# Kernel tuning notes

Measured on AMD Instinct MI355X. Metric: run time of the kernel, lower is better.

## Reference

```python
import jax, jax.numpy as jnp
import numpy as np

B, S, D, H, DFF, K = 16, 1024, 1024, 16, 4096, 3


def setup_inputs() -> dict:
    key = jax.random.key(0)
    ks = jax.random.split(key, 8)
    f = lambda k, sh: jax.random.normal(k, sh, jnp.float32) * 0.02
    return dict(
        x=jax.random.normal(ks[0], (B, S, D), jnp.float32),
        mask=jnp.ones((B, 1, S), jnp.int32),
        alpha1=jnp.ones((D,), jnp.float32), bias1=jnp.zeros((D,), jnp.float32),
        alpha2=jnp.ones((D,), jnp.float32), bias2=jnp.zeros((D,), jnp.float32),
        W_l1=f(ks[1], (D, 2 * D)), b_l1=jnp.zeros((2 * D,), jnp.float32),
        conv_w=f(ks[2], (H, K)),
        W_l2=f(ks[3], (D, D)), b_l2=jnp.zeros((D,), jnp.float32),
        W_ff1=f(ks[4], (D, DFF)), b_ff1=jnp.zeros((DFF,), jnp.float32),
        W_ff2=f(ks[5], (DFF, D)), b_ff2=jnp.zeros((D,), jnp.float32),
    )


def _norm(x, alpha, bias, eps=1e-6):
    # Norm: alpha * (x - mean) / (std + eps) + bias, torch std is unbiased (ddof=1)
    mu = x.mean(-1, keepdims=True)
    sd = x.std(-1, keepdims=True, ddof=1)
    return alpha * (x - mu) / (sd + eps) + bias


def _lightconv(x, conv_w):
    # x: [B, S, C]; conv_w: [H, K] softmax-normalized over K; channels in a head share kernel
    C = x.shape[-1]
    w = jax.nn.softmax(conv_w, axis=-1)              # [H, K]
    wk = jnp.repeat(w, C // H, axis=0)[:, None, :]   # [C, 1, K] depthwise kernel
    y = jax.lax.conv_general_dilated(
        x.transpose(0, 2, 1), wk, (1,), [(K // 2, (K - 1) // 2)],
        dimension_numbers=('NCH', 'OIH', 'NCH'), feature_group_count=C)
    return y.transpose(0, 2, 1)


def reference(x, mask, alpha1, bias1, alpha2, bias2, W_l1, b_l1, conv_w,
              W_l2, b_l2, W_ff1, b_ff1, W_ff2, b_ff2):
    # --- lightweight-conv sublayer ---
    res = x
    h = _norm(x, alpha1, bias1)
    h = h @ W_l1 + b_l1                         # [B,S,2C]
    a, b = jnp.split(h, 2, axis=-1)
    h = a * jax.nn.sigmoid(b)                   # GLU -> [B,S,C]
    cm = mask[:, -1, :][:, :, None]             # [B,S,1]
    h = jnp.where(cm == 0, 0.0, h)
    h = _lightconv(h, conv_w)
    h = h @ W_l2 + b_l2
    x = res + h
    # --- FFN sublayer ---
    res = x
    h = _norm(x, alpha2, bias2)
    h = jax.nn.relu(h @ W_ff1 + b_ff1) @ W_ff2 + b_ff2
    return res + h
```

## Files before the change

kernel.cpp:

```cpp
#include <hip/hip_runtime.h>

typedef unsigned short ushort_t;
typedef __attribute__((ext_vector_type(8))) short s8v;
typedef __attribute__((ext_vector_type(4))) float f4v;

__device__ __forceinline__ float b2f(ushort_t h) {
    union { unsigned u; float f; } c; c.u = ((unsigned)h) << 16; return c.f;
}
__device__ __forceinline__ ushort_t f2b(float f) {
    union { float f; unsigned u; } c; c.f = f;
    unsigned u = c.u;
    return (ushort_t)((u + 0x7fffu + ((u >> 16) & 1u)) >> 16);
}

__device__ __forceinline__ void glds16(const void* g, void* l) {
    __builtin_amdgcn_global_load_lds(
        (const __attribute__((address_space(1))) void*)g,
        (__attribute__((address_space(3))) void*)l, 16, 0, 0);
}

template <int PERM>
__global__ __launch_bounds__(256) void trans_k(const float* __restrict__ W,
                                               ushort_t* __restrict__ Wt,
                                               int K, int N) {
    __shared__ float tile[64][65];
    int k0 = blockIdx.x * 64, n0 = blockIdx.y * 64;
    int t = threadIdx.x;
    int c = t & 63, r4 = t >> 6;
#pragma unroll
    for (int i = 0; i < 16; ++i) {
        int r = i * 4 + r4;
        tile[r][c] = W[(size_t)(k0 + r) * N + n0 + c];
    }
    __syncthreads();
#pragma unroll
    for (int i = 0; i < 16; ++i) {
        int r = i * 4 + r4;
        int s = n0 + r;
        int d;
        if (PERM) {
            int a = (s < 1024);
            int s2 = a ? s : s - 1024;
            d = ((s2 >> 7) << 8) + (a ? 0 : 128) + (s2 & 127);
        } else {
            d = s;
        }
        Wt[(size_t)d * K + k0 + c] = f2b(tile[c][r]);
    }
}

__global__ __launch_bounds__(256) void norm_k(const float* __restrict__ x,
                                              const float* __restrict__ al,
                                              const float* __restrict__ be,
                                              ushort_t* __restrict__ out) {
    int row = blockIdx.x;
    const float4* xr = (const float4*)(x + (size_t)row * 1024);
    float4 v = xr[threadIdx.x];
    float s = v.x + v.y + v.z + v.w;
    float q = v.x * v.x + v.y * v.y + v.z * v.z + v.w * v.w;
#pragma unroll
    for (int o = 32; o > 0; o >>= 1) {
        s += __shfl_down(s, o);
        q += __shfl_down(q, o);
    }
    __shared__ float ss[4], qq[4];
    int lane = threadIdx.x & 63, wv = threadIdx.x >> 6;
    if (lane == 0) { ss[wv] = s; qq[wv] = q; }
    __syncthreads();
    s = ss[0] + ss[1] + ss[2] + ss[3];
    q = qq[0] + qq[1] + qq[2] + qq[3];
    float mu = s * (1.f / 1024.f);
    float var = (q - 1024.f * mu * mu) * (1.f / 1023.f);
    var = fmaxf(var, 0.f);
    float inv = 1.f / (sqrtf(var) + 1e-6f);
    float4 a4 = ((const float4*)al)[threadIdx.x];
    float4 b4 = ((const float4*)be)[threadIdx.x];
    ushort4 o4;
    o4.x = f2b(a4.x * (v.x - mu) * inv + b4.x);
    o4.y = f2b(a4.y * (v.y - mu) * inv + b4.y);
    o4.z = f2b(a4.z * (v.z - mu) * inv + b4.z);
    o4.w = f2b(a4.w * (v.w - mu) * inv + b4.w);
    ((ushort4*)(out + (size_t)row * 1024))[threadIdx.x] = o4;
}

__global__ __launch_bounds__(256) void conv_k(const ushort_t* __restrict__ g,
                                              const float* __restrict__ cw,
                                              ushort_t* __restrict__ out) {
    int i = blockIdx.x * 256 + threadIdx.x;
    int row = i >> 7;
    int cc = (i & 127) << 3;
    int s = row & 1023;
    int head = cc >> 6;
    float w0 = cw[head * 3 + 0], w1 = cw[head * 3 + 1], w2 = cw[head * 3 + 2];
    float mx = fmaxf(w0, fmaxf(w1, w2));
    float e0 = __expf(w0 - mx), e1 = __expf(w1 - mx), e2 = __expf(w2 - mx);
    float inv = 1.f / (e0 + e1 + e2);
    w0 = e0 * inv; w1 = e1 * inv; w2 = e2 * inv;
    size_t base = (size_t)row * 1024 + cc;
    s8v z = {0, 0, 0, 0, 0, 0, 0, 0};
    s8v vm = (s > 0)    ? *(const s8v*)(g + base - 1024) : z;
    s8v v0 = *(const s8v*)(g + base);
    s8v vp = (s < 1023) ? *(const s8v*)(g + base + 1024) : z;
    s8v ov;
#pragma unroll
    for (int j = 0; j < 8; ++j) {
        float r = w0 * b2f((ushort_t)vm[j]) + w1 * b2f((ushort_t)v0[j]) +
                  w2 * b2f((ushort_t)vp[j]);
        ov[j] = (short)f2b(r);
    }
    *(s8v*)(out + base) = ov;
}

template <int EPI>
__global__ __launch_bounds__(512, 1) void gemm_k(const ushort_t* __restrict__ A,
                                                 const ushort_t* __restrict__ Bt,
                                                 const float* __restrict__ bias,
                                                 const int* __restrict__ maskp,
                                                 const float* res, float* outf,
                                                 ushort_t* outb, int N, int K) {
    __shared__ char smem[131072] __attribute__((aligned(128)));
    const int NBN = N >> 8;
    const int per = gridDim.x >> 3;
    const int tt = (blockIdx.x & 7) * per + (blockIdx.x >> 3);
    const int gw = NBN << 3;
    const int g = tt / gw;
    const int rem = tt - g * gw;
    const int bm = (g << 3) + (rem & 7);
    const int bn = rem >> 3;

    const int t = threadIdx.x;
    const int l = t & 63, w = t >> 6;
    const int wm = w >> 2, wn = w & 3;
    const int lr = l & 15, lk = l >> 4;

    const int swzel = (((t & 3) ^ ((t >> 3) & 3)) << 3);
    const int r0 = t >> 2;
    const ushort_t* pA0 = A + (size_t)(bm * 256 + r0) * K + swzel;
    const ushort_t* pA1 = pA0 + (size_t)128 * K;
    const ushort_t* pB0 = Bt + (size_t)(bn * 256 + r0) * K + swzel;
    const ushort_t* pB1 = pB0 + (size_t)128 * K;

    const int fswz = ((lk ^ ((lr >> 1) & 3)) << 4);
    int aoff[8], boff[4];
#pragma unroll
    for (int m = 0; m < 8; ++m)
        aoff[m] = (wm * 128 + m * 16 + lr) * 64 + fswz;
#pragma unroll
    for (int n = 0; n < 4; ++n)
        boff[n] = 16384 + (wn * 64 + n * 16 + lr) * 64 + fswz;

    f4v acc[8][4];
#pragma unroll
    for (int m = 0; m < 8; ++m)
#pragma unroll
        for (int n = 0; n < 4; ++n) acc[m][n] = f4v{0.f, 0.f, 0.f, 0.f};

    const int NK = K >> 5;

#pragma unroll
    for (int p = 0; p < 3; ++p) {
        char* d = smem + p * 32768 + t * 16;
        glds16(pA0 + p * 32, d);
        glds16(pA1 + p * 32, d + 8192);
        glds16(pB0 + p * 32, d + 16384);
        glds16(pB1 + p * 32, d + 24576);
    }
    asm volatile("s_waitcnt vmcnt(8)");
    __builtin_amdgcn_s_barrier();
    __builtin_amdgcn_sched_barrier(0);

    s8v aL0[4], bF0[4], aL1[4], bF1[4], aH[4];
#pragma unroll
    for (int m = 0; m < 4; ++m) aL0[m] = *(const s8v*)(smem + aoff[m]);
#pragma unroll
    for (int n = 0; n < 4; ++n) bF0[n] = *(const s8v*)(smem + boff[n]);

#define KSTEP(I, CAL, CBF, NAL, NBF)                                           \
    {                                                                          \
        const int i_ = (I);                                                    \
        const char* cb_ = smem + (size_t)(i_ & 3) * 32768;                     \
        const char* nb_ = smem + (size_t)((i_ + 1) & 3) * 32768;               \
        int st_ = i_ + 3; if (st_ >= NK) st_ = NK - 1;                         \
        char* sd_ = smem + (size_t)((i_ + 3) & 3) * 32768 + t * 16;            \
        const int ko_ = st_ * 32;                                              \
        _Pragma("unroll")                                                      \
        for (int m = 0; m < 4; ++m) aH[m] = *(const s8v*)(cb_ + aoff[4 + m]);  \
        glds16(pA0 + ko_, sd_);                                                \
        glds16(pA1 + ko_, sd_ + 8192);                                         \
        glds16(pB0 + ko_, sd_ + 16384);                                        \
        glds16(pB1 + ko_, sd_ + 24576);                                        \
        __builtin_amdgcn_s_setprio(1);                                         \
        _Pragma("unroll")                                                      \
        for (int m = 0; m < 4; ++m)                                            \
            _Pragma("unroll")                                                  \
            for (int n = 0; n < 4; ++n)                                        \
                acc[m][n] = __builtin_amdgcn_mfma_f32_16x16x32_bf16(           \
                    CAL[m], CBF[n], acc[m][n], 0, 0, 0);                       \
        __builtin_amdgcn_s_setprio(0);                                         \
        __builtin_amdgcn_sched_barrier(0);                                     \
        asm volatile("s_waitcnt vmcnt(6)");                                    \
        __builtin_amdgcn_s_barrier();                                          \
        __builtin_amdgcn_sched_barrier(0);                                     \
        _Pragma("unroll")                                                      \
        for (int m = 0; m < 4; ++m) NAL[m] = *(const s8v*)(nb_ + aoff[m]);     \
        _Pragma("unroll")                                                      \
        for (int n = 0; n < 4; ++n) NBF[n] = *(const s8v*)(nb_ + boff[n]);     \
        __builtin_amdgcn_s_setprio(1);                                         \
        _Pragma("unroll")                                                      \
        for (int m = 0; m < 4; ++m)                                            \
            _Pragma("unroll")                                                  \
            for (int n = 0; n < 4; ++n)                                        \
                acc[4 + m][n] = __builtin_amdgcn_mfma_f32_16x16x32_bf16(       \
                    aH[m], CBF[n], acc[4 + m][n], 0, 0, 0);                    \
        __builtin_amdgcn_s_setprio(0);                                         \
    }

    for (int ii = 0; ii < NK; ii += 2) {
        KSTEP(ii, aL0, bF0, aL1, bF1);
        KSTEP(ii + 1, aL1, bF1, aL0, bF0);
    }
#undef KSTEP

    if (EPI == 1) {
#pragma unroll
        for (int n = 0; n < 4; ++n) {
            int gcol = bn * 256 + wn * 64 + n * 16 + lr;
            float bb = bias[gcol];
#pragma unroll
            for (int m = 0; m < 8; ++m) {
#pragma unroll
                for (int r = 0; r < 4; ++r) {
                    int grow = bm * 256 + wm * 128 + m * 16 + lk * 4 + r;
                    size_t oi = (size_t)grow * N + gcol;
                    outf[oi] = acc[m][n][r] + bb + res[oi];
                }
            }
        }
    } else {
        asm volatile("s_waitcnt vmcnt(0)" ::: "memory");
        __builtin_amdgcn_s_barrier();
        float bb4[4];
#pragma unroll
        for (int n = 0; n < 4; ++n) {
            int d = bn * 256 + wn * 64 + n * 16 + lr;
            int src = ((d >> 8) << 7) + (d & 127) + (((d >> 7) & 1) << 10);
            bb4[n] = bias[src];
        }
#pragma unroll
        for (int m = 0; m < 8; ++m)
#pragma unroll
            for (int n = 0; n < 4; ++n)
#pragma unroll
                for (int r = 0; r < 4; ++r) {
                    int row = wm * 128 + m * 16 + lk * 4 + r;
                    int colb = ((wn * 64 + n * 16 + lr) * 2) ^ ((row & 3) << 4);
                    *(ushort_t*)(smem + row * 512 + colb) =
                        f2b(acc[m][n][r] + bb4[n]);
                }
        __builtin_amdgcn_s_barrier();
#pragma unroll
        for (int s = 0; s < 8; ++s) {
            int row = s * 32 + (t >> 4);
            int abyt = row * 512 + (((t & 15) * 16) ^ ((row & 3) << 4));
            s8v av = *(const s8v*)(smem + abyt);
            s8v bv = *(const s8v*)(smem + abyt + 256);
            int grow = bm * 256 + row;
            float mval = (maskp[grow] == 0) ? 0.f : 1.f;
            s8v ov;
#pragma unroll
            for (int j = 0; j < 8; ++j) {
                float a = b2f((ushort_t)av[j]);
                float xx = b2f((ushort_t)bv[j]);
                ov[j] = (short)f2b(a * mval / (1.f + __expf(-xx)));
            }
            *(s8v*)(outb + (size_t)grow * (N >> 1) + bn * 128 + (t & 15) * 8) =
                ov;
        }
    }
}

template <int EPI>
__global__ __launch_bounds__(256, 1) void gemm4w_k(
    const ushort_t* __restrict__ A, const ushort_t* __restrict__ Bt,
    const float* __restrict__ bias, const float* res, float* outf,
    ushort_t* outb, int N, int K) {
    __shared__ char smem[131072] __attribute__((aligned(128)));
    const int NBN = N >> 8;
    const int per = gridDim.x >> 3;
    const int tt = (blockIdx.x & 7) * per + (blockIdx.x >> 3);
    const int gw = NBN << 3;
    const int g = tt / gw;
    const int rem = tt - g * gw;
    const int bm = (g << 3) + (rem & 7);
    const int bn = rem >> 3;

    const int t = threadIdx.x;
    const int l = t & 63, w = t >> 6;
    const int wm = w >> 1, wn = w & 1;
    const int lr = l & 15, lk = l >> 4;

    const int swzel = (((t & 3) ^ ((t >> 3) & 3)) << 3);
    const int r0 = t >> 2;
    const ushort_t* pA[4];
    const ushort_t* pB[4];
#pragma unroll
    for (int j = 0; j < 4; ++j) {
        pA[j] = A + (size_t)(bm * 256 + r0 + 64 * j) * K + swzel;
        pB[j] = Bt + (size_t)(bn * 256 + r0 + 64 * j) * K + swzel;
    }

    const int fswz = ((lk ^ ((lr >> 1) & 3)) << 4);
    int aoff[8], boff[8];
#pragma unroll
    for (int m = 0; m < 8; ++m) {
        aoff[m] = (wm * 128 + m * 16 + lr) * 64 + fswz;
        boff[m] = 16384 + (wn * 128 + m * 16 + lr) * 64 + fswz;
    }

    f4v acc[8][8];
#pragma unroll
    for (int m = 0; m < 8; ++m)
#pragma unroll
        for (int n = 0; n < 8; ++n) acc[m][n] = f4v{0.f, 0.f, 0.f, 0.f};

    const int NK = K >> 5;

#pragma unroll
    for (int p = 0; p < 3; ++p) {
        char* d = smem + p * 32768 + t * 16;
#pragma unroll
        for (int j = 0; j < 4; ++j) {
            glds16(pA[j] + p * 32, d + j * 4096);
            glds16(pB[j] + p * 32, d + 16384 + j * 4096);
        }
    }
    asm volatile("s_waitcnt vmcnt(16)");
    __builtin_amdgcn_s_barrier();
    __builtin_amdgcn_sched_barrier(0);

    for (int i = 0; i < NK; ++i) {
        const char* cb = smem + (size_t)(i & 3) * 32768;
        int st = i + 3; if (st >= NK) st = NK - 1;
        const int ko = st * 32;
        char* sd = smem + (size_t)((i + 3) & 3) * 32768 + t * 16;

#pragma unroll
        for (int j = 0; j < 4; ++j) {
            glds16(pA[j] + ko, sd + j * 4096);
            glds16(pB[j] + ko, sd + 16384 + j * 4096);
        }

        s8v aF[8], bF[8];
#pragma unroll
        for (int m = 0; m < 8; ++m) aF[m] = *(const s8v*)(cb + aoff[m]);
#pragma unroll
        for (int n = 0; n < 8; ++n) bF[n] = *(const s8v*)(cb + boff[n]);
        __builtin_amdgcn_s_setprio(1);
#pragma unroll
        for (int m = 0; m < 8; ++m)
#pragma unroll
            for (int n = 0; n < 8; ++n)
                acc[m][n] = __builtin_amdgcn_mfma_f32_16x16x32_bf16(
                    aF[m], bF[n], acc[m][n], 0, 0, 0);
        __builtin_amdgcn_s_setprio(0);

        __builtin_amdgcn_sched_barrier(0);
        asm volatile("s_waitcnt vmcnt(16)");
        __builtin_amdgcn_s_barrier();
        __builtin_amdgcn_sched_barrier(0);
    }

    if (EPI == 1) {
#pragma unroll
        for (int n = 0; n < 8; ++n) {
            int gcol = bn * 256 + wn * 128 + n * 16 + lr;
            float bb = bias[gcol];
#pragma unroll
            for (int m = 0; m < 8; ++m) {
#pragma unroll
                for (int r = 0; r < 4; ++r) {
                    int grow = bm * 256 + wm * 128 + m * 16 + lk * 4 + r;
                    size_t oi = (size_t)grow * N + gcol;
                    outf[oi] = acc[m][n][r] + bb + res[oi];
                }
            }
        }
    } else {
        asm volatile("s_waitcnt vmcnt(0)" ::: "memory");
        __builtin_amdgcn_s_barrier();
        float bb8[8];
#pragma unroll
        for (int n = 0; n < 8; ++n)
            bb8[n] = bias[bn * 256 + wn * 128 + n * 16 + lr];
#pragma unroll
        for (int m = 0; m < 8; ++m)
#pragma unroll
            for (int n = 0; n < 8; ++n)
#pragma unroll
                for (int r = 0; r < 4; ++r) {
                    int row = wm * 128 + m * 16 + lk * 4 + r;
                    int colb =
                        ((wn * 128 + n * 16 + lr) * 2) ^ ((row & 3) << 4);
                    *(ushort_t*)(smem + row * 512 + colb) =
                        f2b(fmaxf(acc[m][n][r] + bb8[n], 0.f));
                }
        __builtin_amdgcn_s_barrier();
#pragma unroll
        for (int s = 0; s < 32; ++s) {
            int row = s * 8 + (t >> 5);
            int byt = row * 512 + (((t & 31) * 16) ^ ((row & 3) << 4));
            int grow = bm * 256 + row;
            int gcol = bn * 256 + (t & 31) * 8;
            *(s8v*)(outb + (size_t)grow * N + gcol) = *(const s8v*)(smem + byt);
        }
    }
}

extern "C" void kernel_launch(void* const* d_in, const int* in_sizes, int n_in,
                              void* d_out, int out_size, void* d_ws, size_t ws_size,
                              hipStream_t stream) {
    const float* x      = (const float*)d_in[0];
    const int*   mask   = (const int*)d_in[1];
    const float* alpha1 = (const float*)d_in[2];
    const float* bias1  = (const float*)d_in[3];
    const float* alpha2 = (const float*)d_in[4];
    const float* bias2  = (const float*)d_in[5];
    const float* W_l1   = (const float*)d_in[6];
    const float* b_l1   = (const float*)d_in[7];
    const float* conv_w = (const float*)d_in[8];
    const float* W_l2   = (const float*)d_in[9];
    const float* b_l2   = (const float*)d_in[10];
    const float* W_ff1  = (const float*)d_in[11];
    const float* b_ff1  = (const float*)d_in[12];
    const float* W_ff2  = (const float*)d_in[13];
    const float* b_ff2  = (const float*)d_in[14];
    float* out = (float*)d_out;

    char* ws = (char*)d_ws;
    size_t off = 0;
    auto alloc = [&](size_t b) {
        char* p = ws + off;
        off += (b + 255) & ~(size_t)255;
        return p;
    };
    ushort_t* Wl1t  = (ushort_t*)alloc(2048ull * 1024 * 2);
    ushort_t* Wl2t  = (ushort_t*)alloc(1024ull * 1024 * 2);
    ushort_t* Wff1t = (ushort_t*)alloc(4096ull * 1024 * 2);
    ushort_t* Wff2t = (ushort_t*)alloc(1024ull * 4096 * 2);
    char* regA = alloc(134217728ull);
    ushort_t* B1 = (ushort_t*)alloc(33554432ull);
    ushort_t* C1 = (ushort_t*)alloc(33554432ull);
    ushort_t* G1 = (ushort_t*)regA;
    ushort_t* f1 = (ushort_t*)regA;

    const int R = 16384;

    trans_k<1><<<dim3(16, 32), 256, 0, stream>>>(W_l1, Wl1t, 1024, 2048);
    trans_k<0><<<dim3(16, 16), 256, 0, stream>>>(W_l2, Wl2t, 1024, 1024);
    trans_k<0><<<dim3(16, 64), 256, 0, stream>>>(W_ff1, Wff1t, 1024, 4096);
    trans_k<0><<<dim3(64, 16), 256, 0, stream>>>(W_ff2, Wff2t, 4096, 1024);

    norm_k<<<R, 256, 0, stream>>>(x, alpha1, bias1, B1);
    gemm_k<3><<<64 * 8, 512, 0, stream>>>(B1, Wl1t, b_l1, mask, nullptr,
                                          nullptr, G1, 2048, 1024);
    conv_k<<<8192, 256, 0, stream>>>(G1, conv_w, C1);
    gemm_k<1><<<64 * 4, 512, 0, stream>>>(C1, Wl2t, b_l2, nullptr, x, out,
                                          nullptr, 1024, 1024);

    norm_k<<<R, 256, 0, stream>>>(out, alpha2, bias2, B1);
    gemm4w_k<2><<<64 * 16, 256, 0, stream>>>(B1, Wff1t, b_ff1, nullptr,
                                             nullptr, f1, 4096, 1024);
    gemm4w_k<1><<<64 * 4, 256, 0, stream>>>(f1, Wff2t, b_ff2, out, out,
                                            nullptr, 1024, 4096);
}
```

Measured before the change: 609.2 us.

## Rewrite FFN GEMM as 8-wave ping-pong kernel with interleaved loads

```diff
diff --git a/kernel.cpp b/kernel.cpp
--- a/kernel.cpp
+++ b/kernel.cpp
@@ -280,7 +280,7 @@
 }
 
 template <int EPI>
-__global__ __launch_bounds__(256, 1) void gemm4w_k(
+__global__ __launch_bounds__(512, 1) void gemm8p_k(
     const ushort_t* __restrict__ A, const ushort_t* __restrict__ Bt,
     const float* __restrict__ bias, const float* res, float* outf,
     ushort_t* outb, int N, int K) {
@@ -296,90 +296,153 @@
 
     const int t = threadIdx.x;
     const int l = t & 63, w = t >> 6;
-    const int wm = w >> 1, wn = w & 1;
+    const int wm = w >> 2, wn = w & 3;
     const int lr = l & 15, lk = l >> 4;
-
-    const int swzel = (((t & 3) ^ ((t >> 3) & 3)) << 3);
-    const int r0 = t >> 2;
-    const ushort_t* pA[4];
-    const ushort_t* pB[4];
-#pragma unroll
-    for (int j = 0; j < 4; ++j) {
-        pA[j] = A + (size_t)(bm * 256 + r0 + 64 * j) * K + swzel;
-        pB[j] = Bt + (size_t)(bn * 256 + r0 + 64 * j) * K + swzel;
-    }
-
-    const int fswz = ((lk ^ ((lr >> 1) & 3)) << 4);
-    int aoff[8], boff[8];
-#pragma unroll
-    for (int m = 0; m < 8; ++m) {
-        aoff[m] = (wm * 128 + m * 16 + lr) * 64 + fswz;
-        boff[m] = 16384 + (wn * 128 + m * 16 + lr) * 64 + fswz;
-    }
-
-    f4v acc[8][8];
+    const int t16 = t * 16;
+
+    const int srcsl = (((t & 7) ^ ((t >> 3) & 7)) << 3);
+    const int rs = t >> 3;
+    const ushort_t* pAL0 = A + (size_t)(bm * 256 + rs) * K + srcsl;
+    const ushort_t* pAL1 = pAL0 + (size_t)64 * K;
+    const ushort_t* pAH0 = pAL0 + (size_t)128 * K;
+    const ushort_t* pAH1 = pAL0 + (size_t)192 * K;
+    const ushort_t* pBL0 = Bt + (size_t)(bn * 256 + rs) * K + srcsl;
+    const ushort_t* pBL1 = pBL0 + (size_t)64 * K;
+    const ushort_t* pBH0 = pBL0 + (size_t)128 * K;
+    const ushort_t* pBH1 = pBL0 + (size_t)192 * K;
+
+    const int rowA = (wm * 16 + lr) * 128;
+    const int rowB = (wn * 16 + lr) * 128;
+    int xk[2];
+#pragma unroll
+    for (int ks = 0; ks < 2; ++ks)
+        xk[ks] = (((ks * 4 + lk) ^ (lr & 7)) << 4);
+
+    f4v acc[8][4];
 #pragma unroll
     for (int m = 0; m < 8; ++m)
 #pragma unroll
-        for (int n = 0; n < 8; ++n) acc[m][n] = f4v{0.f, 0.f, 0.f, 0.f};
-
-    const int NK = K >> 5;
-
-#pragma unroll
-    for (int p = 0; p < 3; ++p) {
-        char* d = smem + p * 32768 + t * 16;
-#pragma unroll
-        for (int j = 0; j < 4; ++j) {
-            glds16(pA[j] + p * 32, d + j * 4096);
-            glds16(pB[j] + p * 32, d + 16384 + j * 4096);
-        }
-    }
-    asm volatile("s_waitcnt vmcnt(16)");
+        for (int n = 0; n < 4; ++n) acc[m][n] = f4v{0.f, 0.f, 0.f, 0.f};
+
+    const int NT = K >> 6;
+
+#pragma unroll
+    for (int p = 0; p < 2; ++p) {
+        char* b = smem + p * 65536 + t16;
+        const int ko = p * 64;
+        glds16(pAL0 + ko, b);
+        glds16(pAL1 + ko, b + 8192);
+        glds16(pBL0 + ko, b + 32768);
+        glds16(pBL1 + ko, b + 40960);
+        glds16(pBH0 + ko, b + 49152);
+        glds16(pBH1 + ko, b + 57344);
+        glds16(pAH0 + ko, b + 16384);
+        glds16(pAH1 + ko, b + 24576);
+    }
+    asm volatile("s_waitcnt vmcnt(8)");
     __builtin_amdgcn_s_barrier();
-    __builtin_amdgcn_sched_barrier(0);
-
-    for (int i = 0; i < NK; ++i) {
-        const char* cb = smem + (size_t)(i & 3) * 32768;
-        int st = i + 3; if (st >= NK) st = NK - 1;
-        const int ko = st * 32;
-        char* sd = smem + (size_t)((i + 3) & 3) * 32768 + t * 16;
-
-#pragma unroll
-        for (int j = 0; j < 4; ++j) {
-            glds16(pA[j] + ko, sd + j * 4096);
-            glds16(pB[j] + ko, sd + 16384 + j * 4096);
-        }
-
-        s8v aF[8], bF[8];
-#pragma unroll
-        for (int m = 0; m < 8; ++m) aF[m] = *(const s8v*)(cb + aoff[m]);
-#pragma unroll
-        for (int n = 0; n < 8; ++n) bF[n] = *(const s8v*)(cb + boff[n]);
-        __builtin_amdgcn_s_setprio(1);
-#pragma unroll
-        for (int m = 0; m < 8; ++m)
-#pragma unroll
-            for (int n = 0; n < 8; ++n)
-                acc[m][n] = __builtin_amdgcn_mfma_f32_16x16x32_bf16(
-                    aF[m], bF[n], acc[m][n], 0, 0, 0);
-        __builtin_amdgcn_s_setprio(0);
-
-        __builtin_amdgcn_sched_barrier(0);
-        asm volatile("s_waitcnt vmcnt(16)");
-        __builtin_amdgcn_s_barrier();
-        __builtin_amdgcn_sched_barrier(0);
-    }
+
+    s8v aR[4][2], bR[4][2];
+
+#define MFMAQ(MB, NB)                                                          \
+    _Pragma("unroll")                                                          \
+    for (int ks = 0; ks < 2; ++ks)                                             \
+        _Pragma("unroll")                                                      \
+        for (int m = 0; m < 4; ++m)                                            \
+            _Pragma("unroll")                                                  \
+            for (int n = 0; n < 2; ++n)                                        \
+                acc[(MB) + m][(NB) + n] =                                      \
+                    __builtin_amdgcn_mfma_f32_16x16x32_bf16(                   \
+                        aR[m][ks], bR[(NB) + n][ks],                           \
+                        acc[(MB) + m][(NB) + n], 0, 0, 0);
+
+#define KT(TI)                                                                 \
+    {                                                                          \
+        const int ti_ = (TI);                                                  \
+        const char* cb_ = smem + (size_t)(ti_ & 1) * 65536;                    \
+        char* sb_ = smem + (size_t)(ti_ & 1) * 65536;                          \
+        int st_ = ti_ + 2;                                                     \
+        if (st_ >= NT) st_ = NT - 2 + (ti_ & 1);                               \
+        const int ko_ = st_ * 64;                                              \
+                                                             \
+        _Pragma("unroll")                                                      \
+        for (int m = 0; m < 4; ++m)                                            \
+            _Pragma("unroll")                                                  \
+            for (int ks = 0; ks < 2; ++ks)                                     \
+                aR[m][ks] = *(const s8v*)(cb_ + m * 4096 + rowA + xk[ks]);     \
+        _Pragma("unroll")                                                      \
+        for (int n = 0; n < 2; ++n)                                            \
+            _Pragma("unroll")                                                  \
+            for (int ks = 0; ks < 2; ++ks)                                     \
+                bR[n][ks] =                                                    \
+                    *(const s8v*)(cb_ + 32768 + n * 8192 + rowB + xk[ks]);     \
+        asm volatile("s_waitcnt lgkmcnt(8)");                                  \
+        __builtin_amdgcn_s_barrier();                                          \
+        asm volatile("s_waitcnt lgkmcnt(0)");                                  \
+        __builtin_amdgcn_s_setprio(1);                                         \
+        MFMAQ(0, 0)                                                            \
+        __builtin_amdgcn_s_setprio(0);                                         \
+        __builtin_amdgcn_s_barrier();                                          \
+                                                             \
+        _Pragma("unroll")                                                      \
+        for (int n = 0; n < 2; ++n)                                            \
+            _Pragma("unroll")                                                  \
+            for (int ks = 0; ks < 2; ++ks)                                     \
+                bR[2 + n][ks] =                                                \
+                    *(const s8v*)(cb_ + 49152 + n * 8192 + rowB + xk[ks]);     \
+        glds16(pAL0 + ko_, sb_ + t16);                                         \
+        glds16(pAL1 + ko_, sb_ + 8192 + t16);                                  \
+        __builtin_amdgcn_s_barrier();                                          \
+        asm volatile("s_waitcnt lgkmcnt(0)");                                  \
+        __builtin_amdgcn_s_setprio(1);                                         \
+        MFMAQ(0, 2)                                                            \
+        __builtin_amdgcn_s_setprio(0);                                         \
+        __builtin_amdgcn_s_barrier();                                          \
+                                                             \
+        _Pragma("unroll")                                                      \
+        for (int m = 0; m < 4; ++m)                                            \
+            _Pragma("unroll")                                                  \
+            for (int ks = 0; ks < 2; ++ks)                                     \
+                aR[m][ks] =                                                    \
+                    *(const s8v*)(cb_ + 16384 + m * 4096 + rowA + xk[ks]);     \
+        glds16(pBL0 + ko_, sb_ + 32768 + t16);                                 \
+        glds16(pBL1 + ko_, sb_ + 40960 + t16);                                 \
+        __builtin_amdgcn_s_barrier();                                          \
+        asm volatile("s_waitcnt lgkmcnt(0)");                                  \
+        __builtin_amdgcn_s_setprio(1);                                         \
+        MFMAQ(4, 0)                                                            \
+        __builtin_amdgcn_s_setprio(0);                                         \
+        __builtin_amdgcn_s_barrier();                                          \
+                                                             \
+        glds16(pBH0 + ko_, sb_ + 49152 + t16);                                 \
+        glds16(pBH1 + ko_, sb_ + 57344 + t16);                                 \
+        glds16(pAH0 + ko_, sb_ + 16384 + t16);                                 \
+        glds16(pAH1 + ko_, sb_ + 24576 + t16);                                 \
+        asm volatile("s_waitcnt vmcnt(6)");                                    \
+        __builtin_amdgcn_s_barrier();                                          \
+        __builtin_amdgcn_s_setprio(1);                                         \
+        MFMAQ(4, 2)                                                            \
+        __builtin_amdgcn_s_setprio(0);                                         \
+        __builtin_amdgcn_s_barrier();                                          \
+    }
+
+    for (int j = 0; j < NT; j += 2) {
+        KT(j);
+        KT(j + 1);
+    }
+#undef KT
+#undef MFMAQ
 
     if (EPI == 1) {
 #pragma unroll
-        for (int n = 0; n < 8; ++n) {
-            int gcol = bn * 256 + wn * 128 + n * 16 + lr;
+        for (int n = 0; n < 4; ++n) {
+            int gcol = bn * 256 + n * 64 + wn * 16 + lr;
             float bb = bias[gcol];
 #pragma unroll
             for (int m = 0; m < 8; ++m) {
 #pragma unroll
                 for (int r = 0; r < 4; ++r) {
-                    int grow = bm * 256 + wm * 128 + m * 16 + lk * 4 + r;
+                    int grow = bm * 256 + m * 32 + wm * 16 + lk * 4 + r;
                     size_t oi = (size_t)grow * N + gcol;
                     outf[oi] = acc[m][n][r] + bb + res[oi];
                 }
@@ -388,26 +451,26 @@
     } else {
         asm volatile("s_waitcnt vmcnt(0)" ::: "memory");
         __builtin_amdgcn_s_barrier();
-        float bb8[8];
-#pragma unroll
-        for (int n = 0; n < 8; ++n)
-            bb8[n] = bias[bn * 256 + wn * 128 + n * 16 + lr];
+        float bb4[4];
+#pragma unroll
+        for (int n = 0; n < 4; ++n)
+            bb4[n] = bias[bn * 256 + n * 64 + wn * 16 + lr];
 #pragma unroll
         for (int m = 0; m < 8; ++m)
 #pragma unroll
-            for (int n = 0; n < 8; ++n)
+            for (int n = 0; n < 4; ++n)
 #pragma unroll
                 for (int r = 0; r < 4; ++r) {
-                    int row = wm * 128 + m * 16 + lk * 4 + r;
+                    int row = m * 32 + wm * 16 + lk * 4 + r;
                     int colb =
-                        ((wn * 128 + n * 16 + lr) * 2) ^ ((row & 3) << 4);
+                        ((n * 64 + wn * 16 + lr) * 2) ^ ((row & 3) << 4);
                     *(ushort_t*)(smem + row * 512 + colb) =
-                        f2b(fmaxf(acc[m][n][r] + bb8[n], 0.f));
+                        f2b(fmaxf(acc[m][n][r] + bb4[n], 0.f));
                 }
         __builtin_amdgcn_s_barrier();
 #pragma unroll
-        for (int s = 0; s < 32; ++s) {
-            int row = s * 8 + (t >> 5);
+        for (int s = 0; s < 16; ++s) {
+            int row = s * 16 + (t >> 5);
             int byt = row * 512 + (((t & 31) * 16) ^ ((row & 3) << 4));
             int grow = bm * 256 + row;
             int gcol = bn * 256 + (t & 31) * 8;
@@ -464,12 +527,12 @@
     gemm_k<3><<<64 * 8, 512, 0, stream>>>(B1, Wl1t, b_l1, mask, nullptr,
                                           nullptr, G1, 2048, 1024);
     conv_k<<<8192, 256, 0, stream>>>(G1, conv_w, C1);
-    gemm_k<1><<<64 * 4, 512, 0, stream>>>(C1, Wl2t, b_l2, nullptr, x, out,
-                                          nullptr, 1024, 1024);
+    gemm8p_k<1><<<64 * 4, 512, 0, stream>>>(C1, Wl2t, b_l2, x, out, nullptr,
+                                            1024, 1024);
 
     norm_k<<<R, 256, 0, stream>>>(out, alpha2, bias2, B1);
-    gemm4w_k<2><<<64 * 16, 256, 0, stream>>>(B1, Wff1t, b_ff1, nullptr,
+    gemm8p_k<2><<<64 * 16, 512, 0, stream>>>(B1, Wff1t, b_ff1, nullptr,
                                              nullptr, f1, 4096, 1024);
-    gemm4w_k<1><<<64 * 4, 256, 0, stream>>>(f1, Wff2t, b_ff2, out, out,
+    gemm8p_k<1><<<64 * 4, 512, 0, stream>>>(f1, Wff2t, b_ff2, out, out,
                                             nullptr, 1024, 4096);
 }
```

Measured after the change: 510.5 us. 1.19x faster.
